# Kernel tuning notes

Hardware: AMD Instinct MI355X
Metric: run time of the kernel (lower is better)

Reference implementation:

```python
import jax, jax.numpy as jnp
import numpy as np

NUM_EMBEDDINGS = 1024
EMBEDDING_DIM = 256
COMMITMENT_COST = 0.25


def setup_inputs() -> dict:
    key = jax.random.key(0)
    k1, k2 = jax.random.split(key)
    inputs = jax.random.normal(k1, (65536, EMBEDDING_DIM), dtype=jnp.float32)
    # original init: uniform(-1/K, 1/K)
    embeddings = jax.random.uniform(
        k2, (NUM_EMBEDDINGS, EMBEDDING_DIM), dtype=jnp.float32,
        minval=-1.0 / NUM_EMBEDDINGS, maxval=1.0 / NUM_EMBEDDINGS)
    return {"inputs": inputs, "embeddings": embeddings}


def reference(inputs, embeddings):
    D = embeddings.shape[1]
    flat = inputs.reshape(-1, D)                                   # [N, D]
    distances = (jnp.sum(flat ** 2, axis=1, keepdims=True)
                 + jnp.sum(embeddings ** 2, axis=1)
                 - 2.0 * flat @ embeddings.T)
    indices = jnp.argmin(distances, axis=1)                        # [N]
    # one-hot @ codebook == direct gather
    quantized = embeddings[indices].reshape(inputs.shape)
    q_loss = jnp.mean((jax.lax.stop_gradient(quantized) - inputs) ** 2)
    e_loss = jnp.mean((quantized - jax.lax.stop_gradient(inputs)) ** 2)
    loss = q_loss + COMMITMENT_COST * e_loss
    # straight-through estimator
    quantized = inputs + jax.lax.stop_gradient(quantized - inputs)
    return quantized, loss
```

## Files before the change

kernel.cpp:

```cpp
#include <hip/hip_runtime.h>
#include <stdint.h>

#define N_ROWS 65536
#define K_CODES 1024
#define DIM 256

typedef unsigned int uint;

#define WS_LOSS_OFF  0
#define WS_ENS_OFF   4096
#define WS_E4_OFF    8192

typedef __attribute__((ext_vector_type(4))) float f32x4;
typedef __attribute__((ext_vector_type(4))) int   i32x4;
typedef __attribute__((ext_vector_type(8))) int   i32x8;

#define XSCALE  (-16.0f)
#define ESCALE4 4096.0f
#define BIAS    16384.0f
#define UNSCALE 3.0517578125e-05f
#define SCALE1  0x7F7F7F7Fu

__device__ __forceinline__ uint pack4_fp8(float a, float b, float c, float d) {
    uint r = 0;
    r = __builtin_amdgcn_cvt_pk_fp8_f32(a, b, r, false);
    r = __builtin_amdgcn_cvt_pk_fp8_f32(c, d, r, true);
    return r;
}
__device__ __forceinline__ uint enc_fp4(float x) {
    float a = fabsf(x);
    uint idx = (a < 0.25f) ? 0u : (a < 0.75f) ? 1u : (a < 1.25f) ? 2u :
               (a < 1.75f) ? 3u : (a < 2.5f)  ? 4u : (a < 3.5f)  ? 5u :
               (a < 5.0f)  ? 6u : 7u;
    return idx | ((x < 0.f) ? 8u : 0u);
}
__device__ __forceinline__ void gload_lds16(const void* g, void* l) {
    __builtin_amdgcn_global_load_lds(
        (const __attribute__((address_space(1))) void*)g,
        (__attribute__((address_space(3))) void*)l, 16, 0, 0);
}

__global__ __launch_bounds__(256) void vq_prep(const float* __restrict__ E,
                                               unsigned char* __restrict__ E4,
                                               float* __restrict__ enS,
                                               float* __restrict__ lossAcc) {
    int id = blockIdx.x * 256 + threadIdx.x;
    if (id == 0) lossAcc[0] = 0.f;
    int code = id >> 6, c4 = id & 63;
    float4 v = *reinterpret_cast<const float4*>(E + (size_t)code * DIM + c4 * 4);
    uint n0 = enc_fp4(v.x * ESCALE4), n1 = enc_fp4(v.y * ESCALE4);
    uint n2 = enc_fp4(v.z * ESCALE4), n3 = enc_fp4(v.w * ESCALE4);
    uint hw = (n0 | (n1 << 4)) | ((n2 | (n3 << 4)) << 8);
    *reinterpret_cast<unsigned short*>(E4 + (size_t)code * 128 + c4 * 2) =
        (unsigned short)hw;

    float s = v.x * v.x + v.y * v.y + v.z * v.z + v.w * v.w;
    #pragma unroll
    for (int m = 32; m >= 1; m >>= 1) s += __shfl_down(s, m, 64);
    if (c4 == 0) enS[code] = s * 32768.0f + BIAS;
}

__global__ __launch_bounds__(256, 2) void vq_main(const float* __restrict__ X,
                                                  const unsigned char* __restrict__ E4,
                                                  const float* __restrict__ enS,
                                                  const float* __restrict__ E,
                                                  float* __restrict__ out,
                                                  float* __restrict__ lossAcc) {
    __shared__ __align__(16) unsigned char bsm[2 * 16384];
    __shared__ float enSLds[1024];
    __shared__ int   bcLds[128];
    __shared__ float lossSh;

    const int tid = threadIdx.x;
    const int lane = tid & 63;
    const int w = tid >> 6;
    const int cl = lane & 15;
    const int kq = lane >> 4;
    const int row0 = blockIdx.x * 128;
    const int key = (cl & 7) << 4;

    auto stageB = [&](int tile, int buf) {
        unsigned char* dst = bsm + buf * 16384;
        const unsigned char* src = E4 + (size_t)(tile * 128) * 128;
        #pragma unroll
        for (int j = 0; j < 4; ++j) {
            int o = j * 4096 + tid * 16;
            int rr = o >> 7;
            int cb = (o & 127) ^ ((rr & 7) << 4);
            gload_lds16(src + rr * 128 + cb, dst + o);
        }
    };

    stageB(0, 0);

    reinterpret_cast<f32x4*>(enSLds)[tid] =
        reinterpret_cast<const f32x4*>(enS)[tid];
    if (tid == 0) lossSh = 0.f;

    i32x8 aF[2][2];
    float xsum = 0.f;
    #pragma unroll
    for (int m = 0; m < 2; ++m) {
        const float* rp = X + (size_t)(row0 + w * 32 + m * 16 + cl) * DIM;
        #pragma unroll
        for (int ks = 0; ks < 2; ++ks) {
            const float* p = rp + ks * 128 + kq * 32;
            uint u[8];
            #pragma unroll
            for (int q = 0; q < 8; ++q) {
                float4 v = *reinterpret_cast<const float4*>(p + q * 4);
                u[q] = pack4_fp8(v.x * XSCALE, v.y * XSCALE,
                                 v.z * XSCALE, v.w * XSCALE);
                xsum = fmaf(v.x, v.x, xsum); xsum = fmaf(v.y, v.y, xsum);
                xsum = fmaf(v.z, v.z, xsum); xsum = fmaf(v.w, v.w, xsum);
            }
            i32x8 f = {(int)u[0], (int)u[1], (int)u[2], (int)u[3],
                       (int)u[4], (int)u[5], (int)u[6], (int)u[7]};
            aF[m][ks] = f;
        }
    }

    uint best[2][4];
    #pragma unroll
    for (int m = 0; m < 2; ++m)
        #pragma unroll
        for (int rr = 0; rr < 4; ++rr) best[m][rr] = 0xFFFFFFFFu;

    for (int t = 0; t < 8; ++t) {
        __syncthreads();
        if (t < 7) stageB(t + 1, (t + 1) & 1);

        const unsigned char* bb = bsm + (t & 1) * 16384;

        f32x4 acc[2][8];
        #pragma unroll
        for (int n = 0; n < 8; ++n) {
            float en = enSLds[t * 128 + n * 16 + cl];
            f32x4 c = {en, en, en, en};
            acc[0][n] = c;
            acc[1][n] = c;
        }

        __builtin_amdgcn_s_setprio(1);
        #pragma unroll
        for (int ks = 0; ks < 2; ++ks) {
            #pragma unroll
            for (int n = 0; n < 8; ++n) {
                const unsigned char* rbase = bb + (size_t)(n * 16 + cl) * 128;
                int l0 = ks * 64 + kq * 16;
                i32x4 lo = *reinterpret_cast<const i32x4*>(rbase + (l0 ^ key));
                i32x8 bf = __builtin_shufflevector(lo, lo, 0, 1, 2, 3, 0, 1, 2, 3);
                #pragma unroll
                for (int m = 0; m < 2; ++m)
                    acc[m][n] = __builtin_amdgcn_mfma_scale_f32_16x16x128_f8f6f4(
                        aF[m][ks], bf, acc[m][n],
                        0, 4,
                        0, SCALE1, 0, SCALE1);
            }
        }
        __builtin_amdgcn_s_setprio(0);

        #pragma unroll
        for (int n = 0; n < 8; ++n) {
            uint codeN = (uint)(t * 128 + n * 16 + cl);
            #pragma unroll
            for (int m = 0; m < 2; ++m)
                #pragma unroll
                for (int rr = 0; rr < 4; ++rr) {
                    uint pk = (__float_as_uint(acc[m][n][rr]) & 0xFFFFFC00u) | codeN;
                    best[m][rr] = min(best[m][rr], pk);
                }
        }
    }

    float minsum = 0.f;
    #pragma unroll
    for (int m = 0; m < 2; ++m)
        #pragma unroll
        for (int rr = 0; rr < 4; ++rr) {
            uint v = best[m][rr];
            #pragma unroll
            for (int mask = 1; mask < 16; mask <<= 1)
                v = min(v, (uint)__shfl_xor((int)v, mask, 64));
            if (cl == 0) {
                int row_l = w * 32 + m * 16 + kq * 4 + rr;
                bcLds[row_l] = (int)(v & 1023u);
                minsum += __uint_as_float(v & 0xFFFFFC00u) - BIAS;
            }
        }
    float v2 = xsum + ((cl == 0) ? minsum * UNSCALE : 0.f);
    #pragma unroll
    for (int mask = 1; mask < 64; mask <<= 1) v2 += __shfl_xor(v2, mask, 64);
    if (lane == 0) atomicAdd(&lossSh, v2);
    __syncthreads();

    #pragma unroll 4
    for (int i = 0; i < 32; ++i) {
        int g = i * 256 + tid;
        int rr = g >> 6, c4 = g & 63;
        int code = bcLds[rr];
        f32x4 q = *reinterpret_cast<const f32x4*>(E + (size_t)code * DIM + c4 * 4);
        __builtin_nontemporal_store(q,
            reinterpret_cast<f32x4*>(out + (size_t)(row0 + rr) * DIM + c4 * 4));
    }
    if (tid == 0) atomicAdd(lossAcc, lossSh);
}

__global__ void vq_finalize(const float* __restrict__ lossAcc,
                            float* __restrict__ out) {
    out[(size_t)N_ROWS * DIM] = 1.25f * lossAcc[0] / (float)((size_t)N_ROWS * DIM);
}

extern "C" void kernel_launch(void* const* d_in, const int* in_sizes, int n_in,
                              void* d_out, int out_size, void* d_ws, size_t ws_size,
                              hipStream_t stream) {
    const float* X = (const float*)d_in[0];
    const float* E = (const float*)d_in[1];
    float* out = (float*)d_out;

    char* ws = (char*)d_ws;
    float* lossAcc = (float*)(ws + WS_LOSS_OFF);
    float* enS = (float*)(ws + WS_ENS_OFF);
    unsigned char* E4 = (unsigned char*)(ws + WS_E4_OFF);

    vq_prep<<<256, 256, 0, stream>>>(E, E4, enS, lossAcc);
    vq_main<<<N_ROWS / 128, 256, 0, stream>>>(X, E4, enS, E, out, lossAcc);
    vq_finalize<<<1, 1, 0, stream>>>(lossAcc, out);
}
```

Measured before the change: 53.81 us.

## Shrink blocks to 64 rows and interleave MFMA with argmin in pairs

Each block now has 2 waves covering 64 rows instead of 4 waves covering 128, and the grid doubles to 1024 blocks. The codebook tile staging is adjusted to the 128-thread block. The inner loop processes code columns in pairs and folds the argmin update in right after each pair, so only 4 accumulators are live instead of 16, which lowers register pressure. The output store also drops the nontemporal hint. Each codebook tile is now staged into LDS for half as many rows, which doubles total staging traffic per row.

```diff
diff --git a/kernel.cpp b/kernel.cpp
--- a/kernel.cpp
+++ b/kernel.cpp
@@ -60,7 +60,7 @@
     if (c4 == 0) enS[code] = s * 32768.0f + BIAS;
 }
 
-__global__ __launch_bounds__(256, 2) void vq_main(const float* __restrict__ X,
+__global__ __launch_bounds__(128, 2) void vq_main(const float* __restrict__ X,
                                                   const unsigned char* __restrict__ E4,
                                                   const float* __restrict__ enS,
                                                   const float* __restrict__ E,
@@ -68,7 +68,7 @@
                                                   float* __restrict__ lossAcc) {
     __shared__ __align__(16) unsigned char bsm[2 * 16384];
     __shared__ float enSLds[1024];
-    __shared__ int   bcLds[128];
+    __shared__ int   bcLds[64];
     __shared__ float lossSh;
 
     const int tid = threadIdx.x;
@@ -76,15 +76,15 @@
     const int w = tid >> 6;
     const int cl = lane & 15;
     const int kq = lane >> 4;
-    const int row0 = blockIdx.x * 128;
+    const int row0 = blockIdx.x * 64;
     const int key = (cl & 7) << 4;
 
     auto stageB = [&](int tile, int buf) {
         unsigned char* dst = bsm + buf * 16384;
         const unsigned char* src = E4 + (size_t)(tile * 128) * 128;
         #pragma unroll
-        for (int j = 0; j < 4; ++j) {
-            int o = j * 4096 + tid * 16;
+        for (int j = 0; j < 8; ++j) {
+            int o = j * 2048 + tid * 16;
             int rr = o >> 7;
             int cb = (o & 127) ^ ((rr & 7) << 4);
             gload_lds16(src + rr * 128 + cb, dst + o);
@@ -93,8 +93,10 @@
 
     stageB(0, 0);
 
-    reinterpret_cast<f32x4*>(enSLds)[tid] =
-        reinterpret_cast<const f32x4*>(enS)[tid];
+    #pragma unroll
+    for (int i = 0; i < 2; ++i)
+        reinterpret_cast<f32x4*>(enSLds)[i * 128 + tid] =
+            reinterpret_cast<const f32x4*>(enS)[i * 128 + tid];
     if (tid == 0) lossSh = 0.f;
 
     i32x8 aF[2][2];
@@ -132,45 +134,48 @@
 
         const unsigned char* bb = bsm + (t & 1) * 16384;
 
-        f32x4 acc[2][8];
-        #pragma unroll
-        for (int n = 0; n < 8; ++n) {
-            float en = enSLds[t * 128 + n * 16 + cl];
-            f32x4 c = {en, en, en, en};
-            acc[0][n] = c;
-            acc[1][n] = c;
-        }
-
         __builtin_amdgcn_s_setprio(1);
         #pragma unroll
-        for (int ks = 0; ks < 2; ++ks) {
-            #pragma unroll
-            for (int n = 0; n < 8; ++n) {
-                const unsigned char* rbase = bb + (size_t)(n * 16 + cl) * 128;
-                int l0 = ks * 64 + kq * 16;
-                i32x4 lo = *reinterpret_cast<const i32x4*>(rbase + (l0 ^ key));
-                i32x8 bf = __builtin_shufflevector(lo, lo, 0, 1, 2, 3, 0, 1, 2, 3);
-                #pragma unroll
-                for (int m = 0; m < 2; ++m)
-                    acc[m][n] = __builtin_amdgcn_mfma_scale_f32_16x16x128_f8f6f4(
-                        aF[m][ks], bf, acc[m][n],
-                        0, 4,
-                        0, SCALE1, 0, SCALE1);
+        for (int np = 0; np < 4; ++np) {
+            const int n0 = np * 2, n1 = np * 2 + 1;
+            float en0 = enSLds[t * 128 + n0 * 16 + cl];
+            float en1 = enSLds[t * 128 + n1 * 16 + cl];
+            f32x4 a00 = {en0, en0, en0, en0};
+            f32x4 a01 = {en1, en1, en1, en1};
+            f32x4 a10 = a00, a11 = a01;
+            const unsigned char* rb0 = bb + (size_t)(n0 * 16 + cl) * 128;
+            const unsigned char* rb1 = bb + (size_t)(n1 * 16 + cl) * 128;
+            #pragma unroll
+            for (int ks = 0; ks < 2; ++ks) {
+                int l0 = (ks * 64 + kq * 16) ^ key;
+                i32x4 lo0 = *reinterpret_cast<const i32x4*>(rb0 + l0);
+                i32x4 lo1 = *reinterpret_cast<const i32x4*>(rb1 + l0);
+                i32x8 bf0 = __builtin_shufflevector(lo0, lo0, 0, 1, 2, 3, 0, 1, 2, 3);
+                i32x8 bf1 = __builtin_shufflevector(lo1, lo1, 0, 1, 2, 3, 0, 1, 2, 3);
+                a00 = __builtin_amdgcn_mfma_scale_f32_16x16x128_f8f6f4(
+                    aF[0][ks], bf0, a00, 0, 4, 0, SCALE1, 0, SCALE1);
+                a10 = __builtin_amdgcn_mfma_scale_f32_16x16x128_f8f6f4(
+                    aF[1][ks], bf0, a10, 0, 4, 0, SCALE1, 0, SCALE1);
+                a01 = __builtin_amdgcn_mfma_scale_f32_16x16x128_f8f6f4(
+                    aF[0][ks], bf1, a01, 0, 4, 0, SCALE1, 0, SCALE1);
+                a11 = __builtin_amdgcn_mfma_scale_f32_16x16x128_f8f6f4(
+                    aF[1][ks], bf1, a11, 0, 4, 0, SCALE1, 0, SCALE1);
+            }
+            uint c0 = (uint)(t * 128 + n0 * 16 + cl);
+            uint c1 = (uint)(t * 128 + n1 * 16 + cl);
+            #pragma unroll
+            for (int rr = 0; rr < 4; ++rr) {
+                best[0][rr] = min(best[0][rr],
+                                  (__float_as_uint(a00[rr]) & 0xFFFFFC00u) | c0);
+                best[0][rr] = min(best[0][rr],
+                                  (__float_as_uint(a01[rr]) & 0xFFFFFC00u) | c1);
+                best[1][rr] = min(best[1][rr],
+                                  (__float_as_uint(a10[rr]) & 0xFFFFFC00u) | c0);
+                best[1][rr] = min(best[1][rr],
+                                  (__float_as_uint(a11[rr]) & 0xFFFFFC00u) | c1);
             }
         }
         __builtin_amdgcn_s_setprio(0);
-
-        #pragma unroll
-        for (int n = 0; n < 8; ++n) {
-            uint codeN = (uint)(t * 128 + n * 16 + cl);
-            #pragma unroll
-            for (int m = 0; m < 2; ++m)
-                #pragma unroll
-                for (int rr = 0; rr < 4; ++rr) {
-                    uint pk = (__float_as_uint(acc[m][n][rr]) & 0xFFFFFC00u) | codeN;
-                    best[m][rr] = min(best[m][rr], pk);
-                }
-        }
     }
 
     float minsum = 0.f;
@@ -196,12 +201,11 @@
 
     #pragma unroll 4
     for (int i = 0; i < 32; ++i) {
-        int g = i * 256 + tid;
+        int g = i * 128 + tid;
         int rr = g >> 6, c4 = g & 63;
         int code = bcLds[rr];
         f32x4 q = *reinterpret_cast<const f32x4*>(E + (size_t)code * DIM + c4 * 4);
-        __builtin_nontemporal_store(q,
-            reinterpret_cast<f32x4*>(out + (size_t)(row0 + rr) * DIM + c4 * 4));
+        *reinterpret_cast<f32x4*>(out + (size_t)(row0 + rr) * DIM + c4 * 4) = q;
     }
     if (tid == 0) atomicAdd(lossAcc, lossSh);
 }
@@ -224,6 +228,6 @@
     unsigned char* E4 = (unsigned char*)(ws + WS_E4_OFF);
 
     vq_prep<<<256, 256, 0, stream>>>(E, E4, enS, lossAcc);
-    vq_main<<<N_ROWS / 128, 256, 0, stream>>>(X, E4, enS, E, out, lossAcc);
+    vq_main<<<N_ROWS / 64, 128, 0, stream>>>(X, E4, enS, E, out, lossAcc);
     vq_finalize<<<1, 1, 0, stream>>>(lossAcc, out);
 }
```

After: 59.50 us. +10.6%, slower.

## Halve rows per block, interleave MFMA with argmin, enlarge LDS to force 1 block/CU

Applied to the files above, without the earlier changes.

Each block now handles 64 rows (16 per wave) instead of 128, so the grid doubles and each wave keeps one A fragment and one accumulator at a time. The distance MFMAs for each code group are fused with the argmin update rather than holding 16 accumulators. The LDS staging buffer is padded to 24KB per stage, the launch bounds drop to 1 block per CU, and the output store is no longer nontemporal. Per block this cuts registers and tail imbalance, but each codebook tile is now reused across half as many rows, doubling codebook LDS traffic per row, and occupancy may fall.

```diff
diff --git a/kernel.cpp b/kernel.cpp
--- a/kernel.cpp
+++ b/kernel.cpp
@@ -60,15 +60,15 @@
     if (c4 == 0) enS[code] = s * 32768.0f + BIAS;
 }
 
-__global__ __launch_bounds__(256, 2) void vq_main(const float* __restrict__ X,
+__global__ __launch_bounds__(256, 1) void vq_main(const float* __restrict__ X,
                                                   const unsigned char* __restrict__ E4,
                                                   const float* __restrict__ enS,
                                                   const float* __restrict__ E,
                                                   float* __restrict__ out,
                                                   float* __restrict__ lossAcc) {
-    __shared__ __align__(16) unsigned char bsm[2 * 16384];
+    __shared__ __align__(16) unsigned char bsm[2 * 24576];
     __shared__ float enSLds[1024];
-    __shared__ int   bcLds[128];
+    __shared__ int   bcLds[64];
     __shared__ float lossSh;
 
     const int tid = threadIdx.x;
@@ -76,11 +76,11 @@
     const int w = tid >> 6;
     const int cl = lane & 15;
     const int kq = lane >> 4;
-    const int row0 = blockIdx.x * 128;
+    const int row0 = blockIdx.x * 64;
     const int key = (cl & 7) << 4;
 
     auto stageB = [&](int tile, int buf) {
-        unsigned char* dst = bsm + buf * 16384;
+        unsigned char* dst = bsm + buf * 24576;
         const unsigned char* src = E4 + (size_t)(tile * 128) * 128;
         #pragma unroll
         for (int j = 0; j < 4; ++j) {
@@ -97,11 +97,10 @@
         reinterpret_cast<const f32x4*>(enS)[tid];
     if (tid == 0) lossSh = 0.f;
 
-    i32x8 aF[2][2];
+    i32x8 aF[2];
     float xsum = 0.f;
-    #pragma unroll
-    for (int m = 0; m < 2; ++m) {
-        const float* rp = X + (size_t)(row0 + w * 32 + m * 16 + cl) * DIM;
+    {
+        const float* rp = X + (size_t)(row0 + w * 16 + cl) * DIM;
         #pragma unroll
         for (int ks = 0; ks < 2; ++ks) {
             const float* p = rp + ks * 128 + kq * 32;
@@ -116,78 +115,57 @@
             }
             i32x8 f = {(int)u[0], (int)u[1], (int)u[2], (int)u[3],
                        (int)u[4], (int)u[5], (int)u[6], (int)u[7]};
-            aF[m][ks] = f;
-        }
-    }
-
-    uint best[2][4];
-    #pragma unroll
-    for (int m = 0; m < 2; ++m)
-        #pragma unroll
-        for (int rr = 0; rr < 4; ++rr) best[m][rr] = 0xFFFFFFFFu;
+            aF[ks] = f;
+        }
+    }
+
+    uint best[4];
+    #pragma unroll
+    for (int rr = 0; rr < 4; ++rr) best[rr] = 0xFFFFFFFFu;
 
     for (int t = 0; t < 8; ++t) {
         __syncthreads();
         if (t < 7) stageB(t + 1, (t + 1) & 1);
 
-        const unsigned char* bb = bsm + (t & 1) * 16384;
-
-        f32x4 acc[2][8];
+        const unsigned char* bb = bsm + (t & 1) * 24576;
+
+        __builtin_amdgcn_s_setprio(1);
         #pragma unroll
         for (int n = 0; n < 8; ++n) {
             float en = enSLds[t * 128 + n * 16 + cl];
-            f32x4 c = {en, en, en, en};
-            acc[0][n] = c;
-            acc[1][n] = c;
-        }
-
-        __builtin_amdgcn_s_setprio(1);
-        #pragma unroll
-        for (int ks = 0; ks < 2; ++ks) {
+            f32x4 acc = {en, en, en, en};
+            const unsigned char* rb = bb + (size_t)(n * 16 + cl) * 128;
             #pragma unroll
-            for (int n = 0; n < 8; ++n) {
-                const unsigned char* rbase = bb + (size_t)(n * 16 + cl) * 128;
-                int l0 = ks * 64 + kq * 16;
-                i32x4 lo = *reinterpret_cast<const i32x4*>(rbase + (l0 ^ key));
+            for (int ks = 0; ks < 2; ++ks) {
+                i32x4 lo = *reinterpret_cast<const i32x4*>(
+                    rb + ((ks * 64 + kq * 16) ^ key));
                 i32x8 bf = __builtin_shufflevector(lo, lo, 0, 1, 2, 3, 0, 1, 2, 3);
-                #pragma unroll
-                for (int m = 0; m < 2; ++m)
-                    acc[m][n] = __builtin_amdgcn_mfma_scale_f32_16x16x128_f8f6f4(
-                        aF[m][ks], bf, acc[m][n],
-                        0, 4,
-                        0, SCALE1, 0, SCALE1);
+                acc = __builtin_amdgcn_mfma_scale_f32_16x16x128_f8f6f4(
+                    aF[ks], bf, acc, 0, 4, 0, SCALE1, 0, SCALE1);
             }
-        }
-        __builtin_amdgcn_s_setprio(0);
-
-        #pragma unroll
-        for (int n = 0; n < 8; ++n) {
             uint codeN = (uint)(t * 128 + n * 16 + cl);
             #pragma unroll
-            for (int m = 0; m < 2; ++m)
-                #pragma unroll
-                for (int rr = 0; rr < 4; ++rr) {
-                    uint pk = (__float_as_uint(acc[m][n][rr]) & 0xFFFFFC00u) | codeN;
-                    best[m][rr] = min(best[m][rr], pk);
-                }
-        }
+            for (int rr = 0; rr < 4; ++rr) {
+                uint pk = (__float_as_uint(acc[rr]) & 0xFFFFFC00u) | codeN;
+                best[rr] = min(best[rr], pk);
+            }
+        }
+        __builtin_amdgcn_s_setprio(0);
     }
 
     float minsum = 0.f;
     #pragma unroll
-    for (int m = 0; m < 2; ++m)
-        #pragma unroll
-        for (int rr = 0; rr < 4; ++rr) {
-            uint v = best[m][rr];
-            #pragma unroll
-            for (int mask = 1; mask < 16; mask <<= 1)
-                v = min(v, (uint)__shfl_xor((int)v, mask, 64));
-            if (cl == 0) {
-                int row_l = w * 32 + m * 16 + kq * 4 + rr;
-                bcLds[row_l] = (int)(v & 1023u);
-                minsum += __uint_as_float(v & 0xFFFFFC00u) - BIAS;
-            }
-        }
+    for (int rr = 0; rr < 4; ++rr) {
+        uint v = best[rr];
+        #pragma unroll
+        for (int mask = 1; mask < 16; mask <<= 1)
+            v = min(v, (uint)__shfl_xor((int)v, mask, 64));
+        if (cl == 0) {
+            int row_l = w * 16 + kq * 4 + rr;
+            bcLds[row_l] = (int)(v & 1023u);
+            minsum += __uint_as_float(v & 0xFFFFFC00u) - BIAS;
+        }
+    }
     float v2 = xsum + ((cl == 0) ? minsum * UNSCALE : 0.f);
     #pragma unroll
     for (int mask = 1; mask < 64; mask <<= 1) v2 += __shfl_xor(v2, mask, 64);
@@ -195,13 +173,12 @@
     __syncthreads();
 
     #pragma unroll 4
-    for (int i = 0; i < 32; ++i) {
+    for (int i = 0; i < 16; ++i) {
         int g = i * 256 + tid;
         int rr = g >> 6, c4 = g & 63;
         int code = bcLds[rr];
         f32x4 q = *reinterpret_cast<const f32x4*>(E + (size_t)code * DIM + c4 * 4);
-        __builtin_nontemporal_store(q,
-            reinterpret_cast<f32x4*>(out + (size_t)(row0 + rr) * DIM + c4 * 4));
+        *reinterpret_cast<f32x4*>(out + (size_t)(row0 + rr) * DIM + c4 * 4) = q;
     }
     if (tid == 0) atomicAdd(lossAcc, lossSh);
 }
@@ -224,6 +201,6 @@
     unsigned char* E4 = (unsigned char*)(ws + WS_E4_OFF);
 
     vq_prep<<<256, 256, 0, stream>>>(E, E4, enS, lossAcc);
-    vq_main<<<N_ROWS / 128, 256, 0, stream>>>(X, E4, enS, E, out, lossAcc);
+    vq_main<<<N_ROWS / 64, 256, 0, stream>>>(X, E4, enS, E, out, lossAcc);
     vq_finalize<<<1, 1, 0, stream>>>(lossAcc, out);
 }
```

Result: slower. 55.75 us (+3.6%).

## Load full FP4 codebook into LDS once per block and drop tile double-buffering

Applied to the files above, without the earlier changes.

Each 512-thread block now stages the whole 128 KB FP4 codebook into LDS at the start, with one barrier, instead of double-buffering 128-code tiles across 8 synchronized iterations. The main loop runs over 64 steps of 16 codes with only two accumulators, which lowers register pressure. Block-level LDS staging of the best index and the loss is replaced by wave shuffles, and each wave does its own global atomic add to the loss. The gather now uses regular stores instead of nontemporal ones. In exchange, only one block fits per CU because of the large LDS footprint. The load-to-compute overlap and the setprio hints are gone, and there are more global atomics.

```diff
diff --git a/kernel.cpp b/kernel.cpp
--- a/kernel.cpp
+++ b/kernel.cpp
@@ -60,42 +60,33 @@
     if (c4 == 0) enS[code] = s * 32768.0f + BIAS;
 }
 
-__global__ __launch_bounds__(256, 2) void vq_main(const float* __restrict__ X,
+__global__ __launch_bounds__(512, 1) void vq_main(const float* __restrict__ X,
                                                   const unsigned char* __restrict__ E4,
                                                   const float* __restrict__ enS,
                                                   const float* __restrict__ E,
                                                   float* __restrict__ out,
                                                   float* __restrict__ lossAcc) {
-    __shared__ __align__(16) unsigned char bsm[2 * 16384];
-    __shared__ float enSLds[1024];
-    __shared__ int   bcLds[128];
-    __shared__ float lossSh;
+    __shared__ __align__(16) unsigned char cbL[131072];
+    __shared__ __align__(16) float enSLds[1024];
 
     const int tid = threadIdx.x;
     const int lane = tid & 63;
     const int w = tid >> 6;
     const int cl = lane & 15;
     const int kq = lane >> 4;
-    const int row0 = blockIdx.x * 128;
+    const int row0 = blockIdx.x * 256;
     const int key = (cl & 7) << 4;
 
-    auto stageB = [&](int tile, int buf) {
-        unsigned char* dst = bsm + buf * 16384;
-        const unsigned char* src = E4 + (size_t)(tile * 128) * 128;
-        #pragma unroll
-        for (int j = 0; j < 4; ++j) {
-            int o = j * 4096 + tid * 16;
-            int rr = o >> 7;
-            int cb = (o & 127) ^ ((rr & 7) << 4);
-            gload_lds16(src + rr * 128 + cb, dst + o);
-        }
-    };
-
-    stageB(0, 0);
-
-    reinterpret_cast<f32x4*>(enSLds)[tid] =
-        reinterpret_cast<const f32x4*>(enS)[tid];
-    if (tid == 0) lossSh = 0.f;
+    #pragma unroll
+    for (int j = 0; j < 16; ++j) {
+        int o = j * 8192 + tid * 16;
+        int rr = o >> 7;
+        int cb = (o & 127) ^ ((rr & 7) << 4);
+        gload_lds16(E4 + (size_t)rr * 128 + cb, cbL + o);
+    }
+    if (tid < 256)
+        reinterpret_cast<f32x4*>(enSLds)[tid] =
+            reinterpret_cast<const f32x4*>(enS)[tid];
 
     i32x8 aF[2][2];
     float xsum = 0.f;
@@ -120,60 +111,42 @@
         }
     }
 
+    __syncthreads();
+
     uint best[2][4];
     #pragma unroll
     for (int m = 0; m < 2; ++m)
         #pragma unroll
         for (int rr = 0; rr < 4; ++rr) best[m][rr] = 0xFFFFFFFFu;
 
-    for (int t = 0; t < 8; ++t) {
-        __syncthreads();
-        if (t < 7) stageB(t + 1, (t + 1) & 1);
-
-        const unsigned char* bb = bsm + (t & 1) * 16384;
-
-        f32x4 acc[2][8];
-        #pragma unroll
-        for (int n = 0; n < 8; ++n) {
-            float en = enSLds[t * 128 + n * 16 + cl];
-            f32x4 c = {en, en, en, en};
-            acc[0][n] = c;
-            acc[1][n] = c;
-        }
-
-        __builtin_amdgcn_s_setprio(1);
+    #pragma unroll 4
+    for (int t = 0; t < 64; ++t) {
+        float en = enSLds[t * 16 + cl];
+        const unsigned char* rb = cbL + (size_t)(t * 16 + cl) * 128;
+        f32x4 acc0 = {en, en, en, en};
+        f32x4 acc1 = acc0;
         #pragma unroll
         for (int ks = 0; ks < 2; ++ks) {
-            #pragma unroll
-            for (int n = 0; n < 8; ++n) {
-                const unsigned char* rbase = bb + (size_t)(n * 16 + cl) * 128;
-                int l0 = ks * 64 + kq * 16;
-                i32x4 lo = *reinterpret_cast<const i32x4*>(rbase + (l0 ^ key));
-                i32x8 bf = __builtin_shufflevector(lo, lo, 0, 1, 2, 3, 0, 1, 2, 3);
-                #pragma unroll
-                for (int m = 0; m < 2; ++m)
-                    acc[m][n] = __builtin_amdgcn_mfma_scale_f32_16x16x128_f8f6f4(
-                        aF[m][ks], bf, acc[m][n],
-                        0, 4,
-                        0, SCALE1, 0, SCALE1);
-            }
+            i32x4 lo = *reinterpret_cast<const i32x4*>(
+                rb + ((ks * 64 + kq * 16) ^ key));
+            i32x8 bf = __builtin_shufflevector(lo, lo, 0, 1, 2, 3, 0, 1, 2, 3);
+            acc0 = __builtin_amdgcn_mfma_scale_f32_16x16x128_f8f6f4(
+                aF[0][ks], bf, acc0, 0, 4, 0, SCALE1, 0, SCALE1);
+            acc1 = __builtin_amdgcn_mfma_scale_f32_16x16x128_f8f6f4(
+                aF[1][ks], bf, acc1, 0, 4, 0, SCALE1, 0, SCALE1);
         }
-        __builtin_amdgcn_s_setprio(0);
-
+        uint codeN = (uint)(t * 16 + cl);
         #pragma unroll
-        for (int n = 0; n < 8; ++n) {
-            uint codeN = (uint)(t * 128 + n * 16 + cl);
-            #pragma unroll
-            for (int m = 0; m < 2; ++m)
-                #pragma unroll
-                for (int rr = 0; rr < 4; ++rr) {
-                    uint pk = (__float_as_uint(acc[m][n][rr]) & 0xFFFFFC00u) | codeN;
-                    best[m][rr] = min(best[m][rr], pk);
-                }
+        for (int rr = 0; rr < 4; ++rr) {
+            best[0][rr] = min(best[0][rr],
+                              (__float_as_uint(acc0[rr]) & 0xFFFFFC00u) | codeN);
+            best[1][rr] = min(best[1][rr],
+                              (__float_as_uint(acc1[rr]) & 0xFFFFFC00u) | codeN);
         }
     }
 
     float minsum = 0.f;
+    int bc[2][4];
     #pragma unroll
     for (int m = 0; m < 2; ++m)
         #pragma unroll
@@ -182,28 +155,23 @@
             #pragma unroll
             for (int mask = 1; mask < 16; mask <<= 1)
                 v = min(v, (uint)__shfl_xor((int)v, mask, 64));
-            if (cl == 0) {
-                int row_l = w * 32 + m * 16 + kq * 4 + rr;
-                bcLds[row_l] = (int)(v & 1023u);
+            bc[m][rr] = (int)(v & 1023u);
+            if (cl == 0)
                 minsum += __uint_as_float(v & 0xFFFFFC00u) - BIAS;
-            }
         }
+
     float v2 = xsum + ((cl == 0) ? minsum * UNSCALE : 0.f);
     #pragma unroll
     for (int mask = 1; mask < 64; mask <<= 1) v2 += __shfl_xor(v2, mask, 64);
-    if (lane == 0) atomicAdd(&lossSh, v2);
-    __syncthreads();
+    if (lane == 0) atomicAdd(lossAcc, v2);
 
-    #pragma unroll 4
+    const int wrow = row0 + w * 32;
+    #pragma unroll
     for (int i = 0; i < 32; ++i) {
-        int g = i * 256 + tid;
-        int rr = g >> 6, c4 = g & 63;
-        int code = bcLds[rr];
-        f32x4 q = *reinterpret_cast<const f32x4*>(E + (size_t)code * DIM + c4 * 4);
-        __builtin_nontemporal_store(q,
-            reinterpret_cast<f32x4*>(out + (size_t)(row0 + rr) * DIM + c4 * 4));
+        int code = __shfl(bc[i >> 4][i & 3], ((i >> 2) & 3) << 4, 64);
+        f32x4 q = *reinterpret_cast<const f32x4*>(E + (size_t)code * DIM + lane * 4);
+        *reinterpret_cast<f32x4*>(out + (size_t)(wrow + i) * DIM + lane * 4) = q;
     }
-    if (tid == 0) atomicAdd(lossAcc, lossSh);
 }
 
 __global__ void vq_finalize(const float* __restrict__ lossAcc,
@@ -224,6 +192,6 @@
     unsigned char* E4 = (unsigned char*)(ws + WS_E4_OFF);
 
     vq_prep<<<256, 256, 0, stream>>>(E, E4, enS, lossAcc);
-    vq_main<<<N_ROWS / 128, 256, 0, stream>>>(X, E4, enS, E, out, lossAcc);
+    vq_main<<<N_ROWS / 256, 512, 0, stream>>>(X, E4, enS, E, out, lossAcc);
     vq_finalize<<<1, 1, 0, stream>>>(lossAcc, out);
 }
```

After: 66.03 us. 1.23x slower.
